# Optimization experiments

Hardware: AMD Instinct MI355X
Metric: run time of the kernel (lower is better)

The kernel has to match this reference:

```python
import jax, jax.numpy as jnp
import numpy as np

E = 1024
H = 8
D = E // H
B = 16384
LN_EPS = 1e-5


def setup_inputs() -> dict:
    key = jax.random.key(0)
    ks = jax.random.split(key, 12)
    s = 1.0 / np.sqrt(E)
    return {
        "image_features": jax.random.normal(ks[0], (B, E), jnp.float32),
        "signal_features": jax.random.normal(ks[1], (B, E), jnp.float32),
        "Wq": jax.random.normal(ks[2], (E, E), jnp.float32) * s,
        "Wk": jax.random.normal(ks[3], (E, E), jnp.float32) * s,
        "Wv": jax.random.normal(ks[4], (E, E), jnp.float32) * s,
        "bq": jnp.zeros((E,), jnp.float32),
        "bk": jnp.zeros((E,), jnp.float32),
        "bv": jnp.zeros((E,), jnp.float32),
        "Wo": jax.random.normal(ks[5], (E, E), jnp.float32) * s,
        "bo": jnp.zeros((E,), jnp.float32),
        "ln_gamma": jnp.ones((E,), jnp.float32),
        "ln_beta": jnp.zeros((E,), jnp.float32),
    }


def _forward(image_features, signal_features, Wq, Wk, Wv, bq, bk, bv, Wo, bo, ln_gamma, ln_beta):
    # query: [B,1,E] from image; key/value: [B,2,E] stacked modalities
    kv = jnp.stack([image_features, signal_features], axis=1)  # [B,2,E]
    # projections (torch Linear convention: x @ W^T + b)
    q = (image_features @ Wq.T + bq).reshape(B, H, 1, D)       # [B,H,1,D]
    k = (kv @ Wk.T + bk).reshape(B, 2, H, D).transpose(0, 2, 1, 3)  # [B,H,2,D]
    v = (kv @ Wv.T + bv).reshape(B, 2, H, D).transpose(0, 2, 1, 3)  # [B,H,2,D]
    scale = 1.0 / jnp.sqrt(jnp.float32(D))
    scores = jnp.einsum("bhqd,bhkd->bhqk", q, k) * scale       # [B,H,1,2]
    attn = jax.nn.softmax(scores, axis=-1)
    ctx = jnp.einsum("bhqk,bhkd->bhqd", attn, v)               # [B,H,1,D]
    ctx = ctx.reshape(B, E)
    attn_out = ctx @ Wo.T + bo
    # residual + LayerNorm (dropout is identity in eval)
    fused = attn_out + image_features
    mu = jnp.mean(fused, axis=-1, keepdims=True)
    var = jnp.var(fused, axis=-1, keepdims=True)
    normed = (fused - mu) * jax.lax.rsqrt(var + LN_EPS)
    return normed * ln_gamma + ln_beta


def reference(image_features, signal_features, Wq, Wk, Wv, bq, bk, bv, Wo, bo, ln_gamma, ln_beta):
    return _forward(image_features, signal_features, Wq, Wk, Wv, bq, bk, bv, Wo, bo, ln_gamma, ln_beta)
```

## Files before the change

kernel.cpp:

```cpp
#include <hip/hip_runtime.h>

#define B_ 16384
#define E_ 1024
#define H_ 8
#define D_ 128

typedef _Float16 f16;
typedef _Float16 f16x8 __attribute__((ext_vector_type(8)));
typedef float f32x4 __attribute__((ext_vector_type(4)));

__device__ __forceinline__ void gload16(const f16* g, f16* l) {
    __builtin_amdgcn_global_load_lds(
        (const __attribute__((address_space(1))) void*)g,
        (__attribute__((address_space(3))) void*)l, 16, 0, 0);
}


__global__ __launch_bounds__(256) void cvt2_kernel(const float4* __restrict__ s0,
                                                   const float4* __restrict__ s1,
                                                   ushort4* __restrict__ d0,
                                                   ushort4* __restrict__ d1, int n4) {
    const float4* s = blockIdx.y ? s1 : s0;
    ushort4* d = blockIdx.y ? d1 : d0;
    int i = blockIdx.x * 256 + threadIdx.x;
    if (i >= n4) return;
    float4 v = s[i];
    union { ushort4 u; f16 h[4]; } o;
    o.h[0] = (f16)v.x; o.h[1] = (f16)v.y; o.h[2] = (f16)v.z; o.h[3] = (f16)v.w;
    d[i] = o.u;
}

__global__ __launch_bounds__(256) void cvt4_kernel(
    const float4* __restrict__ s0, const float4* __restrict__ s1,
    const float4* __restrict__ s2, const float4* __restrict__ s3,
    ushort4* __restrict__ d0, ushort4* __restrict__ d1,
    ushort4* __restrict__ d2, ushort4* __restrict__ d3, int n4) {
    const float4* s; ushort4* d;
    switch (blockIdx.y) {
        case 0: s = s0; d = d0; break;
        case 1: s = s1; d = d1; break;
        case 2: s = s2; d = d2; break;
        default: s = s3; d = d3; break;
    }
    int i = blockIdx.x * 256 + threadIdx.x;
    if (i >= n4) return;
    float4 v = s[i];
    union { ushort4 u; f16 h[4]; } o;
    o.h[0] = (f16)v.x; o.h[1] = (f16)v.y; o.h[2] = (f16)v.z; o.h[3] = (f16)v.w;
    d[i] = o.u;
}

__global__ __launch_bounds__(256, 2) void qkv_attn_kernel(
    const f16* __restrict__ Xi, const f16* __restrict__ Xs,
    const f16* __restrict__ Wq, const f16* __restrict__ Wk, const f16* __restrict__ Wv,
    const float* __restrict__ bq, const float* __restrict__ bk, const float* __restrict__ bv,
    f16* __restrict__ ctx)
{
    __shared__ f16 sAi[2][64][32];
    __shared__ f16 sAs[2][64][32];
    __shared__ f16 sWq[2][128][32];
    __shared__ f16 sWk[2][128][32];
    __shared__ f16 sWv[2][128][32];
    __shared__ float sdot[2][64][2];
    __shared__ float sa0[64];

    const int tid  = threadIdx.x;
    const int lane = tid & 63;
    const int wave = tid >> 6;
    const int wr = wave >> 1, wc = wave & 1;
    const int l16 = lane & 15, lq = lane >> 4;

    const int bid  = blockIdx.x;
    const int head = bid & 7;
    const int row0 = (bid >> 3) * 64;
    const int col0 = head * D_;

    const int lr = lane >> 2;
    const int lc = ((lane & 3) ^ ((lane >> 3) & 3)) * 8;
    const int rc = (lq ^ ((l16 >> 1) & 3)) * 8;

    const f16* gAi = Xi + (size_t)(row0 + wave * 16 + lr) * E_ + lc;
    const f16* gAs = Xs + (size_t)(row0 + wave * 16 + lr) * E_ + lc;
    const size_t woff = (size_t)(col0 + wave * 32 + lr) * E_ + lc;
    const f16* gWq = Wq + woff;
    const f16* gWk = Wk + woff;
    const f16* gWv = Wv + woff;
    const size_t wskip = (size_t)16 * E_;

    f32x4 zero4 = {0.f, 0.f, 0.f, 0.f};
    f32x4 accQ[2][4], accKi[2][4], accKs[2][4], accVi[2][4], accVs[2][4];
    #pragma unroll
    for (int i = 0; i < 2; i++)
        #pragma unroll
        for (int j = 0; j < 4; j++) {
            accQ[i][j] = zero4; accKi[i][j] = zero4; accKs[i][j] = zero4;
            accVi[i][j] = zero4; accVs[i][j] = zero4;
        }

    for (int kk = 0; kk < E_; kk += 64) {
        #pragma unroll
        for (int h = 0; h < 2; h++) {
            const int ko = kk + h * 32;
            gload16(gAi + ko,         &sAi[h][wave * 16][0]);
            gload16(gAs + ko,         &sAs[h][wave * 16][0]);
            gload16(gWq + ko,         &sWq[h][wave * 32][0]);
            gload16(gWq + wskip + ko, &sWq[h][wave * 32 + 16][0]);
            gload16(gWk + ko,         &sWk[h][wave * 32][0]);
            gload16(gWk + wskip + ko, &sWk[h][wave * 32 + 16][0]);
            gload16(gWv + ko,         &sWv[h][wave * 32][0]);
            gload16(gWv + wskip + ko, &sWv[h][wave * 32 + 16][0]);
        }
        __syncthreads();

        #pragma unroll
        for (int h = 0; h < 2; h++) {
            f16x8 aI[2], aS[2], bF[4];
            #pragma unroll
            for (int fr = 0; fr < 2; fr++) {
                aI[fr] = *(const f16x8*)&sAi[h][wr * 32 + fr * 16 + l16][rc];
                aS[fr] = *(const f16x8*)&sAs[h][wr * 32 + fr * 16 + l16][rc];
            }
            #pragma unroll
            for (int fc = 0; fc < 4; fc++)
                bF[fc] = *(const f16x8*)&sWq[h][wc * 64 + fc * 16 + l16][rc];
            #pragma unroll
            for (int fr = 0; fr < 2; fr++)
                #pragma unroll
                for (int fc = 0; fc < 4; fc++)
                    accQ[fr][fc] = __builtin_amdgcn_mfma_f32_16x16x32_f16(aI[fr], bF[fc], accQ[fr][fc], 0, 0, 0);
            #pragma unroll
            for (int fc = 0; fc < 4; fc++)
                bF[fc] = *(const f16x8*)&sWk[h][wc * 64 + fc * 16 + l16][rc];
            #pragma unroll
            for (int fr = 0; fr < 2; fr++)
                #pragma unroll
                for (int fc = 0; fc < 4; fc++) {
                    accKi[fr][fc] = __builtin_amdgcn_mfma_f32_16x16x32_f16(aI[fr], bF[fc], accKi[fr][fc], 0, 0, 0);
                    accKs[fr][fc] = __builtin_amdgcn_mfma_f32_16x16x32_f16(aS[fr], bF[fc], accKs[fr][fc], 0, 0, 0);
                }
            #pragma unroll
            for (int fc = 0; fc < 4; fc++)
                bF[fc] = *(const f16x8*)&sWv[h][wc * 64 + fc * 16 + l16][rc];
            #pragma unroll
            for (int fr = 0; fr < 2; fr++)
                #pragma unroll
                for (int fc = 0; fc < 4; fc++) {
                    accVi[fr][fc] = __builtin_amdgcn_mfma_f32_16x16x32_f16(aI[fr], bF[fc], accVi[fr][fc], 0, 0, 0);
                    accVs[fr][fc] = __builtin_amdgcn_mfma_f32_16x16x32_f16(aS[fr], bF[fc], accVs[fr][fc], 0, 0, 0);
                }
        }
        __syncthreads();
    }

    #pragma unroll
    for (int fc = 0; fc < 4; fc++) {
        int col = col0 + wc * 64 + fc * 16 + l16;
        float bqv = bq[col], bkv = bk[col];
        #pragma unroll
        for (int fr = 0; fr < 2; fr++)
            #pragma unroll
            for (int e = 0; e < 4; e++) {
                accQ[fr][fc][e]  += bqv;
                accKi[fr][fc][e] += bkv;
                accKs[fr][fc][e] += bkv;
            }
    }

    #pragma unroll
    for (int fr = 0; fr < 2; fr++)
        #pragma unroll
        for (int e = 0; e < 4; e++) {
            float d0 = 0.f, d1 = 0.f;
            #pragma unroll
            for (int fc = 0; fc < 4; fc++) {
                d0 += accQ[fr][fc][e] * accKi[fr][fc][e];
                d1 += accQ[fr][fc][e] * accKs[fr][fc][e];
            }
            #pragma unroll
            for (int m = 1; m < 16; m <<= 1) {
                d0 += __shfl_xor(d0, m, 64);
                d1 += __shfl_xor(d1, m, 64);
            }
            if (l16 == 0) {
                int row = wr * 32 + fr * 16 + lq * 4 + e;
                sdot[0][row][wc] = d0;
                sdot[1][row][wc] = d1;
            }
        }
    __syncthreads();
    if (tid < 64) {
        const float scale = 0.088388347648318447f;
        float s0 = (sdot[0][tid][0] + sdot[0][tid][1]) * scale;
        float s1 = (sdot[1][tid][0] + sdot[1][tid][1]) * scale;
        sa0[tid] = 1.0f / (1.0f + expf(s1 - s0));
    }
    __syncthreads();

    #pragma unroll
    for (int fc = 0; fc < 4; fc++) {
        int col = col0 + wc * 64 + fc * 16 + l16;
        float bvv = bv[col];
        #pragma unroll
        for (int fr = 0; fr < 2; fr++)
            #pragma unroll
            for (int e = 0; e < 4; e++) {
                int row = wr * 32 + fr * 16 + lq * 4 + e;
                float a0 = sa0[row];
                float v  = a0 * accVi[fr][fc][e] + (1.0f - a0) * accVs[fr][fc][e] + bvv;
                ctx[(size_t)(row0 + row) * E_ + col] = (f16)v;
            }
    }
}

__global__ __launch_bounds__(256) void out_proj_kernel(
    const f16* __restrict__ A, const f16* __restrict__ Wo, const float* __restrict__ bo,
    f16* __restrict__ a16)
{
    __shared__ f16 sA[2][128][32];
    __shared__ f16 sB[2][128][32];
    const int tid  = threadIdx.x;
    const int lane = tid & 63;
    const int wave = tid >> 6;
    const int wr = wave >> 1, wc = wave & 1;
    const int l16 = lane & 15, lq = lane >> 4;
    const int row0 = blockIdx.x * 128;
    const int col0 = blockIdx.y * 128;

    const int lr = lane >> 2;
    const int lc = ((lane & 3) ^ ((lane >> 3) & 3)) * 8;
    const int rc = (lq ^ ((l16 >> 1) & 3)) * 8;

    const f16* gA0 = A  + (size_t)(row0 + wave * 32 + lr) * E_ + lc;
    const f16* gB0 = Wo + (size_t)(col0 + wave * 32 + lr) * E_ + lc;
    const size_t wskip = (size_t)16 * E_;

    f32x4 zero4 = {0.f, 0.f, 0.f, 0.f};
    f32x4 acc[4][4];
    #pragma unroll
    for (int i = 0; i < 4; i++)
        #pragma unroll
        for (int j = 0; j < 4; j++) acc[i][j] = zero4;

    for (int kk = 0; kk < E_; kk += 64) {
        #pragma unroll
        for (int h = 0; h < 2; h++) {
            const int ko = kk + h * 32;
            gload16(gA0 + ko,         &sA[h][wave * 32][0]);
            gload16(gA0 + wskip + ko, &sA[h][wave * 32 + 16][0]);
            gload16(gB0 + ko,         &sB[h][wave * 32][0]);
            gload16(gB0 + wskip + ko, &sB[h][wave * 32 + 16][0]);
        }
        __syncthreads();

        #pragma unroll
        for (int h = 0; h < 2; h++) {
            f16x8 aF[4], bF[4];
            #pragma unroll
            for (int f = 0; f < 4; f++) {
                aF[f] = *(const f16x8*)&sA[h][wr * 64 + f * 16 + l16][rc];
                bF[f] = *(const f16x8*)&sB[h][wc * 64 + f * 16 + l16][rc];
            }
            #pragma unroll
            for (int fr = 0; fr < 4; fr++)
                #pragma unroll
                for (int fc = 0; fc < 4; fc++)
                    acc[fr][fc] = __builtin_amdgcn_mfma_f32_16x16x32_f16(aF[fr], bF[fc], acc[fr][fc], 0, 0, 0);
        }
        __syncthreads();
    }

    #pragma unroll
    for (int fc = 0; fc < 4; fc++) {
        int col = col0 + wc * 64 + fc * 16 + l16;
        float bov = bo[col];
        #pragma unroll
        for (int fr = 0; fr < 4; fr++)
            #pragma unroll
            for (int e = 0; e < 4; e++) {
                int row = row0 + wr * 64 + fr * 16 + lq * 4 + e;
                a16[(size_t)row * E_ + col] = (f16)(acc[fr][fc][e] + bov);
            }
    }
}

__global__ __launch_bounds__(256) void ln_kernel(
    const f16* __restrict__ a16, const float* __restrict__ resid,
    const float* __restrict__ gamma, const float* __restrict__ beta,
    float* __restrict__ out)
{
    const int row = blockIdx.x;
    const int tid = threadIdx.x;
    union { ushort4 u; f16 h[4]; } ua;
    ua.u = ((const ushort4*)(a16 + (size_t)row * E_))[tid];
    float4 rv = ((const float4*)(resid + (size_t)row * E_))[tid];
    float4 v;
    v.x = (float)ua.h[0] + rv.x;
    v.y = (float)ua.h[1] + rv.y;
    v.z = (float)ua.h[2] + rv.z;
    v.w = (float)ua.h[3] + rv.w;
    float s  = v.x + v.y + v.z + v.w;
    float s2 = v.x * v.x + v.y * v.y + v.z * v.z + v.w * v.w;
    #pragma unroll
    for (int m = 1; m < 64; m <<= 1) {
        s  += __shfl_xor(s, m, 64);
        s2 += __shfl_xor(s2, m, 64);
    }
    __shared__ float red[8];
    int wv = tid >> 6, ln = tid & 63;
    if (ln == 0) { red[wv] = s; red[4 + wv] = s2; }
    __syncthreads();
    s  = red[0] + red[1] + red[2] + red[3];
    s2 = red[4] + red[5] + red[6] + red[7];
    float mu  = s * (1.0f / E_);
    float var = s2 * (1.0f / E_) - mu * mu;
    float r   = rsqrtf(var + 1e-5f);
    float4 g  = ((const float4*)gamma)[tid];
    float4 bb = ((const float4*)beta)[tid];
    float4 o;
    o.x = (v.x - mu) * r * g.x + bb.x;
    o.y = (v.y - mu) * r * g.y + bb.y;
    o.z = (v.z - mu) * r * g.z + bb.z;
    o.w = (v.w - mu) * r * g.w + bb.w;
    ((float4*)(out + (size_t)row * E_))[tid] = o;
}

extern "C" void kernel_launch(void* const* d_in, const int* in_sizes, int n_in,
                              void* d_out, int out_size, void* d_ws, size_t ws_size,
                              hipStream_t stream)
{
    (void)in_sizes; (void)n_in; (void)out_size; (void)ws_size;
    const float* image  = (const float*)d_in[0];
    const float* signal = (const float*)d_in[1];
    const float* Wq = (const float*)d_in[2];
    const float* Wk = (const float*)d_in[3];
    const float* Wv = (const float*)d_in[4];
    const float* bq = (const float*)d_in[5];
    const float* bk = (const float*)d_in[6];
    const float* bv = (const float*)d_in[7];
    const float* Wo = (const float*)d_in[8];
    const float* bo = (const float*)d_in[9];
    const float* gamma = (const float*)d_in[10];
    const float* beta  = (const float*)d_in[11];
    float* out = (float*)d_out;

    char* ws = (char*)d_ws;
    f16* Xi16 = (f16*)(ws);
    f16* Xs16 = (f16*)(ws + 32ull * 1024 * 1024);
    f16* Wq16 = (f16*)(ws + 64ull * 1024 * 1024);
    f16* Wk16 = (f16*)(ws + 66ull * 1024 * 1024);
    f16* Wv16 = (f16*)(ws + 68ull * 1024 * 1024);
    f16* Wo16 = (f16*)(ws + 70ull * 1024 * 1024);
    f16* ctx  = (f16*)(ws + 72ull * 1024 * 1024);
    f16* a16  = Xi16;

    const int nBE4 = B_ * E_ / 4;
    const int nEE4 = E_ * E_ / 4;
    dim3 gX(nBE4 / 256, 2);
    cvt2_kernel<<<gX, 256, 0, stream>>>((const float4*)image, (const float4*)signal,
                                        (ushort4*)Xi16, (ushort4*)Xs16, nBE4);
    dim3 gW(nEE4 / 256, 4);
    cvt4_kernel<<<gW, 256, 0, stream>>>((const float4*)Wq, (const float4*)Wk,
                                        (const float4*)Wv, (const float4*)Wo,
                                        (ushort4*)Wq16, (ushort4*)Wk16,
                                        (ushort4*)Wv16, (ushort4*)Wo16, nEE4);

    qkv_attn_kernel<<<B_ / 64 * H_, 256, 0, stream>>>(Xi16, Xs16, Wq16, Wk16, Wv16,
                                                      bq, bk, bv, ctx);

    dim3 g4(B_ / 128, E_ / 128);
    out_proj_kernel<<<g4, 256, 0, stream>>>(ctx, Wo16, bo, a16);

    ln_kernel<<<B_, 256, 0, stream>>>(a16, image, gamma, beta, out);
}
```

Baseline: 444.3 us.

## Enlarge out-projection tile to 256x128, remap grid, read fp16 residual in LayerNorm

The output-projection GEMM tile grows from 128x128 to 256x128, with each wave computing 64 rows by all 128 columns. This raises MFMA work per LDS load, and a 1D grid with column-fastest ordering lets neighbouring blocks share A rows in cache. The LayerNorm kernel now reads the residual from the fp16 copy of image features instead of fp32, so the out-projection result goes into the signal buffer. This halves residual read traffic but makes the residual add less precise, and the larger accumulator array increases register pressure.

After: 440.0 us. No clear change (-1.0%).

```diff
diff --git a/kernel.cpp b/kernel.cpp
--- a/kernel.cpp
+++ b/kernel.cpp
@@ -212,92 +212,96 @@
     }
 }
 
-__global__ __launch_bounds__(256) void out_proj_kernel(
+__global__ __launch_bounds__(256, 2) void out_proj_kernel(
     const f16* __restrict__ A, const f16* __restrict__ Wo, const float* __restrict__ bo,
     f16* __restrict__ a16)
 {
-    __shared__ f16 sA[2][128][32];
+    __shared__ f16 sA[2][256][32];
     __shared__ f16 sB[2][128][32];
     const int tid  = threadIdx.x;
     const int lane = tid & 63;
     const int wave = tid >> 6;
-    const int wr = wave >> 1, wc = wave & 1;
     const int l16 = lane & 15, lq = lane >> 4;
-    const int row0 = blockIdx.x * 128;
-    const int col0 = blockIdx.y * 128;
+
+    const int bid  = blockIdx.x;
+    const int col0 = (bid & 7) * 128;
+    const int row0 = (bid >> 3) * 256;
 
     const int lr = lane >> 2;
     const int lc = ((lane & 3) ^ ((lane >> 3) & 3)) * 8;
     const int rc = (lq ^ ((l16 >> 1) & 3)) * 8;
 
-    const f16* gA0 = A  + (size_t)(row0 + wave * 32 + lr) * E_ + lc;
+    const f16* gA0 = A  + (size_t)(row0 + wave * 64 + lr) * E_ + lc;
     const f16* gB0 = Wo + (size_t)(col0 + wave * 32 + lr) * E_ + lc;
-    const size_t wskip = (size_t)16 * E_;
+    const size_t rskip = (size_t)16 * E_;
 
     f32x4 zero4 = {0.f, 0.f, 0.f, 0.f};
-    f32x4 acc[4][4];
+    f32x4 acc[4][8];
     #pragma unroll
     for (int i = 0; i < 4; i++)
         #pragma unroll
-        for (int j = 0; j < 4; j++) acc[i][j] = zero4;
+        for (int j = 0; j < 8; j++) acc[i][j] = zero4;
 
     for (int kk = 0; kk < E_; kk += 64) {
         #pragma unroll
         for (int h = 0; h < 2; h++) {
             const int ko = kk + h * 32;
-            gload16(gA0 + ko,         &sA[h][wave * 32][0]);
-            gload16(gA0 + wskip + ko, &sA[h][wave * 32 + 16][0]);
-            gload16(gB0 + ko,         &sB[h][wave * 32][0]);
-            gload16(gB0 + wskip + ko, &sB[h][wave * 32 + 16][0]);
+            #pragma unroll
+            for (int j = 0; j < 4; j++)
+                gload16(gA0 + (size_t)j * rskip + ko, &sA[h][wave * 64 + j * 16][0]);
+            #pragma unroll
+            for (int j = 0; j < 2; j++)
+                gload16(gB0 + (size_t)j * rskip + ko, &sB[h][wave * 32 + j * 16][0]);
         }
         __syncthreads();
 
         #pragma unroll
         for (int h = 0; h < 2; h++) {
-            f16x8 aF[4], bF[4];
-            #pragma unroll
-            for (int f = 0; f < 4; f++) {
-                aF[f] = *(const f16x8*)&sA[h][wr * 64 + f * 16 + l16][rc];
-                bF[f] = *(const f16x8*)&sB[h][wc * 64 + f * 16 + l16][rc];
-            }
+            f16x8 aF[4], bF[8];
+            #pragma unroll
+            for (int f = 0; f < 4; f++)
+                aF[f] = *(const f16x8*)&sA[h][wave * 64 + f * 16 + l16][rc];
+            #pragma unroll
+            for (int g = 0; g < 8; g++)
+                bF[g] = *(const f16x8*)&sB[h][g * 16 + l16][rc];
             #pragma unroll
             for (int fr = 0; fr < 4; fr++)
                 #pragma unroll
-                for (int fc = 0; fc < 4; fc++)
+                for (int fc = 0; fc < 8; fc++)
                     acc[fr][fc] = __builtin_amdgcn_mfma_f32_16x16x32_f16(aF[fr], bF[fc], acc[fr][fc], 0, 0, 0);
         }
         __syncthreads();
     }
 
     #pragma unroll
-    for (int fc = 0; fc < 4; fc++) {
-        int col = col0 + wc * 64 + fc * 16 + l16;
+    for (int fc = 0; fc < 8; fc++) {
+        int col = col0 + fc * 16 + l16;
         float bov = bo[col];
         #pragma unroll
         for (int fr = 0; fr < 4; fr++)
             #pragma unroll
             for (int e = 0; e < 4; e++) {
-                int row = row0 + wr * 64 + fr * 16 + lq * 4 + e;
+                int row = row0 + wave * 64 + fr * 16 + lq * 4 + e;
                 a16[(size_t)row * E_ + col] = (f16)(acc[fr][fc][e] + bov);
             }
     }
 }
 
 __global__ __launch_bounds__(256) void ln_kernel(
-    const f16* __restrict__ a16, const float* __restrict__ resid,
+    const f16* __restrict__ a16, const f16* __restrict__ resid16,
     const float* __restrict__ gamma, const float* __restrict__ beta,
     float* __restrict__ out)
 {
     const int row = blockIdx.x;
     const int tid = threadIdx.x;
-    union { ushort4 u; f16 h[4]; } ua;
-    ua.u = ((const ushort4*)(a16 + (size_t)row * E_))[tid];
-    float4 rv = ((const float4*)(resid + (size_t)row * E_))[tid];
+    union { ushort4 u; f16 h[4]; } ua, ur;
+    ua.u = ((const ushort4*)(a16     + (size_t)row * E_))[tid];
+    ur.u = ((const ushort4*)(resid16 + (size_t)row * E_))[tid];
     float4 v;
-    v.x = (float)ua.h[0] + rv.x;
-    v.y = (float)ua.h[1] + rv.y;
-    v.z = (float)ua.h[2] + rv.z;
-    v.w = (float)ua.h[3] + rv.w;
+    v.x = (float)ua.h[0] + (float)ur.h[0];
+    v.y = (float)ua.h[1] + (float)ur.h[1];
+    v.z = (float)ua.h[2] + (float)ur.h[2];
+    v.w = (float)ua.h[3] + (float)ur.h[3];
     float s  = v.x + v.y + v.z + v.w;
     float s2 = v.x * v.x + v.y * v.y + v.z * v.z + v.w * v.w;
     #pragma unroll
@@ -351,7 +355,7 @@
     f16* Wv16 = (f16*)(ws + 68ull * 1024 * 1024);
     f16* Wo16 = (f16*)(ws + 70ull * 1024 * 1024);
     f16* ctx  = (f16*)(ws + 72ull * 1024 * 1024);
-    f16* a16  = Xi16;
+    f16* a16  = Xs16;
 
     const int nBE4 = B_ * E_ / 4;
     const int nEE4 = E_ * E_ / 4;
@@ -367,8 +371,7 @@
     qkv_attn_kernel<<<B_ / 64 * H_, 256, 0, stream>>>(Xi16, Xs16, Wq16, Wk16, Wv16,
                                                       bq, bk, bv, ctx);
 
-    dim3 g4(B_ / 128, E_ / 128);
-    out_proj_kernel<<<g4, 256, 0, stream>>>(ctx, Wo16, bo, a16);
-
-    ln_kernel<<<B_, 256, 0, stream>>>(a16, image, gamma, beta, out);
-}
+    out_proj_kernel<<<B_ / 256 * 8, 256, 0, stream>>>(ctx, Wo16, bo, a16);
+
+    ln_kernel<<<B_, 256, 0, stream>>>(a16, Xi16, gamma, beta, out);
+}
```
